# Kernel tuning notes

Hardware: AMD Instinct MI355X
Metric: run time of the kernel (lower is better)

The kernel has to match this reference:

```python
import jax, jax.numpy as jnp
import numpy as np

N = 100000
E = 1600000
IN, HID, OUT = 128, 256, 47


def _glorot(key, shape):
    fan_in, fan_out = shape
    lim = np.sqrt(6.0 / (fan_in + fan_out))
    return jax.random.uniform(key, shape, jnp.float32, -lim, lim)


def setup_inputs() -> dict:
    key = jax.random.key(0)
    ks = jax.random.split(key, 12)
    x = jax.random.normal(ks[0], (N, IN), jnp.float32)
    src = jax.random.randint(ks[1], (E,), 0, N, jnp.int32)
    dst = jax.random.randint(ks[2], (E,), 0, N, jnp.int32)
    dims = [(IN, HID), (HID, HID), (HID, OUT)]
    inp = {"x": x, "src": src, "dst": dst}
    for i, (di, do) in enumerate(dims, 1):
        inp[f"w_self{i}"] = _glorot(ks[2 + 3 * i - 2], (di, do))
        inp[f"w_neigh{i}"] = _glorot(ks[2 + 3 * i - 1], (di, do))
        inp[f"b{i}"] = jnp.zeros((do,), jnp.float32)
    return inp


def sage_conv(x, src, dst, w_self, w_neigh, b):
    n = x.shape[0]
    msg = x[src]                                              # [E, d] gather
    summed = jax.ops.segment_sum(msg, dst, num_segments=n)    # [N, d]
    deg = jax.ops.segment_sum(jnp.ones((src.shape[0],), x.dtype), dst, num_segments=n)
    h_neigh = summed / jnp.maximum(deg, 1.0)[:, None]         # mean aggregate
    return x @ w_self + h_neigh @ w_neigh + b


def reference(x, src, dst, w_self1, w_neigh1, b1, w_self2, w_neigh2, b2, w_self3, w_neigh3, b3):
    h = sage_conv(x, src, dst, w_self1, w_neigh1, b1)
    h = jax.nn.relu(h)  # dropout = identity in eval mode
    h = sage_conv(h, src, dst, w_self2, w_neigh2, b2)
    h = jax.nn.relu(h)
    h = sage_conv(h, src, dst, w_self3, w_neigh3, b3)
    return h
```

## Files before the change

kernel.cpp:

```cpp
#include <hip/hip_runtime.h>

#define N_NODES 100000
#define N_EDGES 1600000

typedef __attribute__((ext_vector_type(8))) _Float16 half8;
typedef __attribute__((ext_vector_type(4))) _Float16 half4v;
typedef __attribute__((ext_vector_type(4))) float floatx4;


__global__ void deg_rank(const int* __restrict__ dst, int* __restrict__ deg,
                         int* __restrict__ rank, int e) {
    int i = blockIdx.x * blockDim.x + threadIdx.x;
    if (i < e) rank[i] = atomicAdd(&deg[dst[i]], 1);
}


__global__ __launch_bounds__(256) void scan_partial(const int* __restrict__ deg,
                                                    int* __restrict__ bsum, int n) {
    __shared__ int wsum[4];
    int t = threadIdx.x;
    int base = blockIdx.x * 2048 + t * 8;
    int tsum = 0;
    #pragma unroll
    for (int k = 0; k < 8; ++k) {
        int idx = base + k;
        tsum += (idx < n) ? deg[idx] : 0;
    }
    #pragma unroll
    for (int d = 1; d < 64; d <<= 1) tsum += __shfl_xor(tsum, d, 64);
    if ((t & 63) == 0) wsum[t >> 6] = tsum;
    __syncthreads();
    if (t == 0) bsum[blockIdx.x] = wsum[0] + wsum[1] + wsum[2] + wsum[3];
}

__global__ void scan_blocksums(const int* __restrict__ bsum, int* __restrict__ bbase, int nb) {
    int t = threadIdx.x;
    int v = (t < nb) ? bsum[t] : 0;
    int s = v;
    #pragma unroll
    for (int d = 1; d < 64; d <<= 1) {
        int u = __shfl_up(s, d, 64);
        if (t >= d) s += u;
    }
    if (t < nb) bbase[t] = s - v;
    if (t == 63) bbase[nb] = s;
}

__global__ __launch_bounds__(256) void scan_write(const int* __restrict__ deg,
                                                  const int* __restrict__ bbase,
                                                  int* __restrict__ offs, int n, int nb) {
    __shared__ int wsum[4];
    int t = threadIdx.x;
    int lane = t & 63, w = t >> 6;
    int base = blockIdx.x * 2048 + t * 8;
    int v[8];
    #pragma unroll
    for (int k = 0; k < 8; ++k) {
        int idx = base + k;
        v[k] = (idx < n) ? deg[idx] : 0;
    }
    int tsum = 0;
    #pragma unroll
    for (int k = 0; k < 8; ++k) { int x = v[k]; v[k] = tsum; tsum += x; }
    int s = tsum;
    #pragma unroll
    for (int d = 1; d < 64; d <<= 1) {
        int u = __shfl_up(s, d, 64);
        if (lane >= d) s += u;
    }
    if (lane == 63) wsum[w] = s;
    __syncthreads();
    int wb = 0;
    for (int j = 0; j < w; ++j) wb += wsum[j];
    int texcl = bbase[blockIdx.x] + wb + (s - tsum);
    #pragma unroll
    for (int k = 0; k < 8; ++k) {
        int idx = base + k;
        if (idx < n) offs[idx] = texcl + v[k];
    }
    if (blockIdx.x == 0 && t == 0) offs[n] = bbase[nb];
}

__global__ void fill_csr2(const int* __restrict__ src, const int* __restrict__ dst,
                          const int* __restrict__ offs, const int* __restrict__ rank,
                          int* __restrict__ csr, int e) {
    int i = blockIdx.x * blockDim.x + threadIdx.x;
    if (i < e) csr[offs[dst[i]] + rank[i]] = src[i];
}


__global__ void cvt_f16(const float4* __restrict__ in, half4v* __restrict__ oh, int n4) {
    int i = blockIdx.x * blockDim.x + threadIdx.x;
    if (i >= n4) return;
    float4 v = in[i];
    half4v h;
    h[0] = (_Float16)v.x; h[1] = (_Float16)v.y;
    h[2] = (_Float16)v.z; h[3] = (_Float16)v.w;
    oh[i] = h;
}


__global__ void prep_all(const float* __restrict__ ws1, const float* __restrict__ wn1,
                         const float* __restrict__ ws2, const float* __restrict__ wn2,
                         const float* __restrict__ ws3, const float* __restrict__ wn3,
                         _Float16* __restrict__ o1s, _Float16* __restrict__ o1n,
                         _Float16* __restrict__ o2s, _Float16* __restrict__ o2n,
                         _Float16* __restrict__ o3c) {
    int i = blockIdx.x * blockDim.x + threadIdx.x;
    if (i < 65536) {
        const float* W = (i < 32768) ? ws1 : wn1;
        _Float16* O = (i < 32768) ? o1s : o1n;
        int j = i & 32767;
        int nn = j >> 7, k = j & 127;
        O[j] = (_Float16)W[k * 256 + nn];
    } else if (i < 196608) {
        int j = i - 65536;
        const float* W = (j < 65536) ? ws2 : wn2;
        _Float16* O = (j < 65536) ? o2s : o2n;
        j &= 65535;
        int nn = j >> 8, k = j & 255;
        O[j] = (_Float16)W[k * 256 + nn];
    } else if (i < 221184) {
        int j = i - 196608;
        const float* W = (j < 12288) ? ws3 : wn3;
        _Float16* O = o3c + ((j < 12288) ? 0 : 12288);
        j = (j < 12288) ? j : j - 12288;
        int nn = j >> 8, k = j & 255;
        O[j] = (nn < 47) ? (_Float16)W[k * 47 + nn] : (_Float16)0.f;
    }
}


__global__ __launch_bounds__(256) void aggP(const _Float16* __restrict__ Xp,
                                            const int* __restrict__ csr,
                                            const int* __restrict__ offs,
                                            _Float16* __restrict__ Pp, int n) {
    int node = blockIdx.x * 4 + (threadIdx.x >> 6);
    int lane = threadIdx.x & 63;
    int qtr = lane >> 4;
    int sl = lane & 15;
    if (node >= n) return;
    int e0 = offs[node], e1 = offs[node + 1];
    float a[8] = {0.f, 0.f, 0.f, 0.f, 0.f, 0.f, 0.f, 0.f};
    int e = e0;
    for (; e + 16 <= e1; e += 16) {
        int s0 = csr[e + qtr];
        int s1 = csr[e + 4 + qtr];
        int s2 = csr[e + 8 + qtr];
        int s3 = csr[e + 12 + qtr];
        half8 u0 = ((const half8*)(Xp + (size_t)s0 * 128))[sl];
        half8 u1 = ((const half8*)(Xp + (size_t)s1 * 128))[sl];
        half8 u2 = ((const half8*)(Xp + (size_t)s2 * 128))[sl];
        half8 u3 = ((const half8*)(Xp + (size_t)s3 * 128))[sl];
        #pragma unroll
        for (int j = 0; j < 8; ++j) a[j] += (float)u0[j];
        #pragma unroll
        for (int j = 0; j < 8; ++j) a[j] += (float)u1[j];
        #pragma unroll
        for (int j = 0; j < 8; ++j) a[j] += (float)u2[j];
        #pragma unroll
        for (int j = 0; j < 8; ++j) a[j] += (float)u3[j];
    }
    for (; e + 8 <= e1; e += 8) {
        int s0 = csr[e + qtr];
        int s1 = csr[e + 4 + qtr];
        half8 u0 = ((const half8*)(Xp + (size_t)s0 * 128))[sl];
        half8 u1 = ((const half8*)(Xp + (size_t)s1 * 128))[sl];
        #pragma unroll
        for (int j = 0; j < 8; ++j) a[j] += (float)u0[j];
        #pragma unroll
        for (int j = 0; j < 8; ++j) a[j] += (float)u1[j];
    }
    for (; e + 4 <= e1; e += 4) {
        int s = csr[e + qtr];
        half8 u = ((const half8*)(Xp + (size_t)s * 128))[sl];
        #pragma unroll
        for (int j = 0; j < 8; ++j) a[j] += (float)u[j];
    }
    int rem = e1 - e;
    if (qtr < rem) {
        int s = csr[e + qtr];
        half8 u = ((const half8*)(Xp + (size_t)s * 128))[sl];
        #pragma unroll
        for (int j = 0; j < 8; ++j) a[j] += (float)u[j];
    }
    #pragma unroll
    for (int j = 0; j < 8; ++j) {
        a[j] += __shfl_xor(a[j], 16);
        a[j] += __shfl_xor(a[j], 32);
    }
    if (lane < 16) {
        float inv = 1.0f / fmaxf((float)(e1 - e0), 1.0f);
        half8 rh;
        #pragma unroll
        for (int j = 0; j < 8; ++j) rh[j] = (_Float16)(a[j] * inv);
        ((half8*)(Pp + (size_t)node * 128))[sl] = rh;
    }
}

__global__ __launch_bounds__(256) void agg_l3(const _Float16* __restrict__ Y,
                                              const float* __restrict__ S,
                                              const int* __restrict__ csr,
                                              const int* __restrict__ offs,
                                              float* __restrict__ out, int n) {
    int node = blockIdx.x * 4 + (threadIdx.x >> 6);
    int lane = threadIdx.x & 63;
    int qtr = lane >> 4;
    int sl = lane & 15;
    int c = sl < 12 ? sl : 11;
    if (node >= n) return;
    int e0 = offs[node], e1 = offs[node + 1];
    float a0 = 0.f, a1 = 0.f, a2 = 0.f, a3 = 0.f;
    int e = e0;
    for (; e + 8 <= e1; e += 8) {
        int s0 = csr[e + qtr];
        int s1 = csr[e + 4 + qtr];
        half4v f0 = ((const half4v*)(Y + (size_t)s0 * 48))[c];
        half4v f1 = ((const half4v*)(Y + (size_t)s1 * 48))[c];
        a0 += (float)f0[0] + (float)f1[0];
        a1 += (float)f0[1] + (float)f1[1];
        a2 += (float)f0[2] + (float)f1[2];
        a3 += (float)f0[3] + (float)f1[3];
    }
    for (; e + 4 <= e1; e += 4) {
        int s = csr[e + qtr];
        half4v f = ((const half4v*)(Y + (size_t)s * 48))[c];
        a0 += (float)f[0]; a1 += (float)f[1]; a2 += (float)f[2]; a3 += (float)f[3];
    }
    int rem = e1 - e;
    if (qtr < rem) {
        int s = csr[e + qtr];
        half4v f = ((const half4v*)(Y + (size_t)s * 48))[c];
        a0 += (float)f[0]; a1 += (float)f[1]; a2 += (float)f[2]; a3 += (float)f[3];
    }
    a0 += __shfl_xor(a0, 16); a0 += __shfl_xor(a0, 32);
    a1 += __shfl_xor(a1, 16); a1 += __shfl_xor(a1, 32);
    a2 += __shfl_xor(a2, 16); a2 += __shfl_xor(a2, 32);
    a3 += __shfl_xor(a3, 16); a3 += __shfl_xor(a3, 32);
    if (lane < 12) {
        float inv = 1.0f / fmaxf((float)(e1 - e0), 1.0f);
        float4 sv = ((const float4*)(S + (size_t)node * 48))[c];
        float r[4] = {sv.x + a0 * inv, sv.y + a1 * inv, sv.z + a2 * inv, sv.w + a3 * inv};
        #pragma unroll
        for (int k = 0; k < 4; ++k) {
            int col = c * 4 + k;
            if (col < 47) out[(size_t)node * 47 + col] = r[k];
        }
    }
}


template <int NTILES, int OUTFMT>
__global__ __launch_bounds__(256, 2) void gemm_mfma(
    const _Float16* __restrict__ A1h, const _Float16* __restrict__ A2h,
    const _Float16* __restrict__ W1, const _Float16* __restrict__ W2,
    const float* __restrict__ bias, float* __restrict__ outS, _Float16* __restrict__ outY,
    _Float16* __restrict__ outh, int n, int K, int dout, int relu, int phases) {
    constexpr int NPAD = NTILES * 16;
    constexpr int LDT = 36;
    __shared__ _Float16 Bs[2][NPAD * LDT];

    const int t = threadIdx.x;
    const int bm = blockIdx.x * 128;
    const int lane = t & 63;
    const int w = t >> 6;
    const int quad = lane >> 4;
    const int tl = lane & 15;
    const int r0 = bm + w * 32 + tl;
    const int r1 = r0 + 16;
    const size_t PS = (size_t)n * 128;

    floatx4 acc[2][NTILES];
    #pragma unroll
    for (int i = 0; i < 2; ++i)
        #pragma unroll
        for (int j = 0; j < NTILES; ++j) acc[i][j] = (floatx4){0.f, 0.f, 0.f, 0.f};

    const int spp = K >> 5;
    const int nsteps = phases * spp;

    half8 pb0, pb1, pb2, pb3;
    half8 a0A = {0}, a1A = {0}, a0B = {0}, a1B = {0};

    auto wload = [&](int s2) {
        int ph2 = (s2 >= spp) ? 1 : 0;
        int k02 = (ph2 ? s2 - spp : s2) << 5;
        const _Float16* W = ph2 ? W2 : W1;
        const half8* p = (const half8*)(W + (size_t)t * K + k02);
        pb0 = p[0]; pb1 = p[1]; pb2 = p[2]; pb3 = p[3];
    };
    auto aload = [&](int s2, half8& d0, half8& d1) {
        int ph2 = (s2 >= spp) ? 1 : 0;
        int k02 = (ph2 ? s2 - spp : s2) << 5;
        const _Float16* Ah = ph2 ? A2h : A1h;
        int kq = k02 + quad * 8;
        const _Float16* Ab = Ah + ((kq >> 7) ? PS : (size_t)0) + (kq & 127);
        d0 = (half8){0}; d1 = (half8){0};
        if (r0 < n) d0 = *(const half8*)(Ab + (size_t)r0 * 128);
        if (r1 < n) d1 = *(const half8*)(Ab + (size_t)r1 * 128);
    };

    if (t < NPAD) {
        wload(0);
        *(half8*)&Bs[0][t * LDT + 0]  = pb0;
        *(half8*)&Bs[0][t * LDT + 8]  = pb1;
        *(half8*)&Bs[0][t * LDT + 16] = pb2;
        *(half8*)&Bs[0][t * LDT + 24] = pb3;
        wload(1);
    }
    aload(0, a0A, a1A);
    aload(1, a0B, a1B);
    __syncthreads();

    for (int s = 0; s < nsteps; s += 2) {
        {
            if (s + 1 < nsteps && t < NPAD) {
                *(half8*)&Bs[1][t * LDT + 0]  = pb0;
                *(half8*)&Bs[1][t * LDT + 8]  = pb1;
                *(half8*)&Bs[1][t * LDT + 16] = pb2;
                *(half8*)&Bs[1][t * LDT + 24] = pb3;
                if (s + 2 < nsteps) wload(s + 2);
            }
            half8 ca0 = a0A, ca1 = a1A;
            if (s + 2 < nsteps) aload(s + 2, a0A, a1A);
            #pragma unroll
            for (int nt = 0; nt < NTILES; ++nt) {
                half8 bh = *(const half8*)&Bs[0][(nt * 16 + tl) * LDT + quad * 8];
                acc[0][nt] = __builtin_amdgcn_mfma_f32_16x16x32_f16(ca0, bh, acc[0][nt], 0, 0, 0);
                acc[1][nt] = __builtin_amdgcn_mfma_f32_16x16x32_f16(ca1, bh, acc[1][nt], 0, 0, 0);
            }
            asm volatile("s_waitcnt lgkmcnt(0)" ::: "memory");
            __builtin_amdgcn_sched_barrier(0);
            __builtin_amdgcn_s_barrier();
        }
        {
            int s1 = s + 1;
            if (s1 + 1 < nsteps && t < NPAD) {
                *(half8*)&Bs[0][t * LDT + 0]  = pb0;
                *(half8*)&Bs[0][t * LDT + 8]  = pb1;
                *(half8*)&Bs[0][t * LDT + 16] = pb2;
                *(half8*)&Bs[0][t * LDT + 24] = pb3;
                if (s1 + 2 < nsteps) wload(s1 + 2);
            }
            half8 ca0 = a0B, ca1 = a1B;
            if (s1 + 2 < nsteps) aload(s1 + 2, a0B, a1B);
            #pragma unroll
            for (int nt = 0; nt < NTILES; ++nt) {
                half8 bh = *(const half8*)&Bs[1][(nt * 16 + tl) * LDT + quad * 8];
                acc[0][nt] = __builtin_amdgcn_mfma_f32_16x16x32_f16(ca0, bh, acc[0][nt], 0, 0, 0);
                acc[1][nt] = __builtin_amdgcn_mfma_f32_16x16x32_f16(ca1, bh, acc[1][nt], 0, 0, 0);
            }
            asm volatile("s_waitcnt lgkmcnt(0)" ::: "memory");
            __builtin_amdgcn_sched_barrier(0);
            __builtin_amdgcn_s_barrier();
        }
    }

    #pragma unroll
    for (int mt = 0; mt < 2; ++mt) {
        #pragma unroll
        for (int nt = 0; nt < NTILES; ++nt) {
            int gc = nt * 16 + tl;
            if (OUTFMT == 1 && gc >= dout) continue;
            #pragma unroll
            for (int r = 0; r < 4; ++r) {
                int gr = bm + w * 32 + mt * 16 + quad * 4 + r;
                if (gr >= n) continue;
                float v = acc[mt][nt][r];
                if (OUTFMT == 1) {
                    v += bias[gc];
                    if (relu) v = fmaxf(v, 0.f);
                    outh[(size_t)(gc >> 7) * PS + (size_t)gr * 128 + (gc & 127)] = (_Float16)v;
                } else {
                    if (gc < 48) {
                        v += (gc < 47) ? bias[gc] : 0.f;
                        outS[(size_t)gr * 48 + gc] = v;
                    } else {
                        outY[(size_t)gr * 48 + (gc - 48)] = (_Float16)v;
                    }
                }
            }
        }
    }
}

extern "C" void kernel_launch(void* const* d_in, const int* in_sizes, int n_in,
                              void* d_out, int out_size, void* d_ws, size_t ws_size,
                              hipStream_t stream) {
    (void)in_sizes; (void)n_in; (void)out_size; (void)ws_size;
    const int N = N_NODES, E = N_EDGES;
    const float* x = (const float*)d_in[0];
    const int* src = (const int*)d_in[1];
    const int* dst = (const int*)d_in[2];
    const float* w_self1 = (const float*)d_in[3];
    const float* w_neigh1 = (const float*)d_in[4];
    const float* b1 = (const float*)d_in[5];
    const float* w_self2 = (const float*)d_in[6];
    const float* w_neigh2 = (const float*)d_in[7];
    const float* b2 = (const float*)d_in[8];
    const float* w_self3 = (const float*)d_in[9];
    const float* w_neigh3 = (const float*)d_in[10];
    const float* b3 = (const float*)d_in[11];
    float* out = (float*)d_out;

    _Float16* Ph = (_Float16*)d_ws;
    _Float16* Hh = Ph + (size_t)N * 256;
    int* deg = (int*)(Hh + (size_t)N * 256);
    int* offs = deg + N;
    int* csr = offs + N + 4;
    _Float16* wbuf = (_Float16*)(csr + E);
    _Float16* w1s = wbuf;
    _Float16* w1n = w1s + 32768;
    _Float16* w2s = w1n + 32768;
    _Float16* w2n = w2s + 65536;
    _Float16* w3c = w2n + 65536;
    int* bsum = (int*)(w3c + 24576);
    int* bbase = bsum + 64;
    int* rank = (int*)Ph;
    _Float16* xh = Ph + (size_t)N * 128;
    float* S = (float*)Ph;
    _Float16* Y = (_Float16*)(S + (size_t)N * 48);

    const int NB = (N + 2047) / 2048;

    hipMemsetAsync(deg, 0, N * sizeof(int), stream);
    deg_rank<<<(E + 255) / 256, 256, 0, stream>>>(dst, deg, rank, E);
    scan_partial<<<NB, 256, 0, stream>>>(deg, bsum, N);
    scan_blocksums<<<1, 64, 0, stream>>>(bsum, bbase, NB);
    scan_write<<<NB, 256, 0, stream>>>(deg, bbase, offs, N, NB);
    fill_csr2<<<(E + 255) / 256, 256, 0, stream>>>(src, dst, offs, rank, csr, E);

    cvt_f16<<<(N * 128 / 4 + 255) / 256, 256, 0, stream>>>((const float4*)x, (half4v*)xh,
                                                           N * 128 / 4);
    prep_all<<<(221184 + 255) / 256, 256, 0, stream>>>(w_self1, w_neigh1, w_self2, w_neigh2,
                                                       w_self3, w_neigh3, w1s, w1n, w2s, w2n,
                                                       w3c);

    int gemmGrid = (N + 127) / 128;
    int aggGrid = (N + 3) / 4;

    aggP<<<aggGrid, 256, 0, stream>>>(xh, csr, offs, Ph, N);
    gemm_mfma<16, 1><<<gemmGrid, 256, 0, stream>>>(xh, Ph, w1s, w1n, b1, nullptr, nullptr,
                                                   Hh, N, 128, 256, 1, 2);
    aggP<<<aggGrid, 256, 0, stream>>>(Hh, csr, offs, Ph, N);
    aggP<<<aggGrid, 256, 0, stream>>>(Hh + (size_t)N * 128, csr, offs, Ph + (size_t)N * 128, N);
    gemm_mfma<16, 1><<<gemmGrid, 256, 0, stream>>>(Hh, Ph, w2s, w2n, b2, nullptr, nullptr,
                                                   Hh, N, 256, 256, 1, 2);
    gemm_mfma<6, 2><<<gemmGrid, 256, 0, stream>>>(Hh, nullptr, w3c, nullptr, b3, S, Y,
                                                  nullptr, N, 256, 96, 0, 1);
    agg_l3<<<aggGrid, 256, 0, stream>>>(Y, S, csr, offs, out, N);
}
```

Measured before the change: 643.7 us.

## Add 64-row GEMM kernel with column-split grid and separate layer-2 output buffer

Adds a new MFMA GEMM kernel that tiles 64 rows per block and splits the output columns across a second grid dimension, so there are more, smaller blocks and a higher occupancy target. Layers 1 and 3 use it. For layer 2 it writes to a separate H2 buffer when the workspace is large enough, because column-split blocks cannot safely overwrite their own input in place. Otherwise it falls back to the old in-place kernel. The trade-off is that A tiles are re-read once per column split and fewer MFMAs are issued per A load.

New measurement: 601.0 us. 1.07x faster.

```diff
diff --git a/kernel.cpp b/kernel.cpp
--- a/kernel.cpp
+++ b/kernel.cpp
@@ -13,7 +13,6 @@
     int i = blockIdx.x * blockDim.x + threadIdx.x;
     if (i < e) rank[i] = atomicAdd(&deg[dst[i]], 1);
 }
-
 
 __global__ __launch_bounds__(256) void scan_partial(const int* __restrict__ deg,
                                                     int* __restrict__ bsum, int n) {
@@ -251,6 +250,130 @@
 
 
 template <int NTILES, int OUTFMT>
+__global__ __launch_bounds__(256, 3) void gemm64(
+    const _Float16* __restrict__ A1h, const _Float16* __restrict__ A2h,
+    const _Float16* __restrict__ W1, const _Float16* __restrict__ W2,
+    const float* __restrict__ bias, float* __restrict__ outS, _Float16* __restrict__ outY,
+    _Float16* __restrict__ outh, int n, int K, int relu, int phases) {
+    constexpr int NPAD = NTILES * 16;
+    constexpr int LDT = 36;
+    __shared__ _Float16 Bs[2][NPAD * LDT];
+
+    const int t = threadIdx.x;
+    const int bm = blockIdx.x * 64;
+    const int colbase = blockIdx.y * NPAD;
+    const int lane = t & 63;
+    const int w = t >> 6;
+    const int quad = lane >> 4;
+    const int tl = lane & 15;
+    const int r0 = bm + w * 16 + tl;
+    const size_t PS = (size_t)n * 128;
+
+    floatx4 acc[NTILES];
+    #pragma unroll
+    for (int j = 0; j < NTILES; ++j) acc[j] = (floatx4){0.f, 0.f, 0.f, 0.f};
+
+    const int spp = K >> 5;
+    const int nsteps = phases * spp;
+
+    const int tr = t >> 1;
+    const int koff = (t & 1) * 16;
+    const bool stager = (t < 2 * NPAD);
+
+    half8 pb0, pb1;
+    half8 aA = {0}, aB = {0};
+
+    auto wload = [&](int s2) {
+        int ph2 = (s2 >= spp) ? 1 : 0;
+        int k02 = (ph2 ? s2 - spp : s2) << 5;
+        const _Float16* W = ph2 ? W2 : W1;
+        const half8* p = (const half8*)(W + (size_t)(colbase + tr) * K + k02 + koff);
+        pb0 = p[0]; pb1 = p[1];
+    };
+    auto aload = [&](int s2, half8& d) {
+        int ph2 = (s2 >= spp) ? 1 : 0;
+        int k02 = (ph2 ? s2 - spp : s2) << 5;
+        const _Float16* Ah = ph2 ? A2h : A1h;
+        int kq = k02 + quad * 8;
+        const _Float16* Ab = Ah + ((kq >> 7) ? PS : (size_t)0) + (kq & 127);
+        d = (half8){0};
+        if (r0 < n) d = *(const half8*)(Ab + (size_t)r0 * 128);
+    };
+
+    if (stager) {
+        wload(0);
+        *(half8*)&Bs[0][tr * LDT + koff]     = pb0;
+        *(half8*)&Bs[0][tr * LDT + koff + 8] = pb1;
+        wload(1);
+    }
+    aload(0, aA);
+    aload(1, aB);
+    __syncthreads();
+
+    for (int s = 0; s < nsteps; s += 2) {
+        {
+            if (s + 1 < nsteps && stager) {
+                *(half8*)&Bs[1][tr * LDT + koff]     = pb0;
+                *(half8*)&Bs[1][tr * LDT + koff + 8] = pb1;
+                if (s + 2 < nsteps) wload(s + 2);
+            }
+            half8 ca = aA;
+            if (s + 2 < nsteps) aload(s + 2, aA);
+            #pragma unroll
+            for (int nt = 0; nt < NTILES; ++nt) {
+                half8 bh = *(const half8*)&Bs[0][(nt * 16 + tl) * LDT + quad * 8];
+                acc[nt] = __builtin_amdgcn_mfma_f32_16x16x32_f16(ca, bh, acc[nt], 0, 0, 0);
+            }
+            asm volatile("s_waitcnt lgkmcnt(0)" ::: "memory");
+            __builtin_amdgcn_sched_barrier(0);
+            __builtin_amdgcn_s_barrier();
+        }
+        {
+            int s1 = s + 1;
+            if (s1 + 1 < nsteps && stager) {
+                *(half8*)&Bs[0][tr * LDT + koff]     = pb0;
+                *(half8*)&Bs[0][tr * LDT + koff + 8] = pb1;
+                if (s1 + 2 < nsteps) wload(s1 + 2);
+            }
+            half8 ca = aB;
+            if (s1 + 2 < nsteps) aload(s1 + 2, aB);
+            #pragma unroll
+            for (int nt = 0; nt < NTILES; ++nt) {
+                half8 bh = *(const half8*)&Bs[1][(nt * 16 + tl) * LDT + quad * 8];
+                acc[nt] = __builtin_amdgcn_mfma_f32_16x16x32_f16(ca, bh, acc[nt], 0, 0, 0);
+            }
+            asm volatile("s_waitcnt lgkmcnt(0)" ::: "memory");
+            __builtin_amdgcn_sched_barrier(0);
+            __builtin_amdgcn_s_barrier();
+        }
+    }
+
+    #pragma unroll
+    for (int nt = 0; nt < NTILES; ++nt) {
+        int gc = colbase + nt * 16 + tl;
+        #pragma unroll
+        for (int r = 0; r < 4; ++r) {
+            int gr = bm + w * 16 + quad * 4 + r;
+            if (gr >= n) continue;
+            float v = acc[nt][r];
+            if (OUTFMT == 1) {
+                v += bias[gc];
+                if (relu) v = fmaxf(v, 0.f);
+                outh[(size_t)(gc >> 7) * PS + (size_t)gr * 128 + (gc & 127)] = (_Float16)v;
+            } else {
+                if (gc < 48) {
+                    v += (gc < 47) ? bias[gc] : 0.f;
+                    outS[(size_t)gr * 48 + gc] = v;
+                } else {
+                    outY[(size_t)gr * 48 + (gc - 48)] = (_Float16)v;
+                }
+            }
+        }
+    }
+}
+
+
+template <int NTILES, int OUTFMT>
 __global__ __launch_bounds__(256, 2) void gemm_mfma(
     const _Float16* __restrict__ A1h, const _Float16* __restrict__ A2h,
     const _Float16* __restrict__ W1, const _Float16* __restrict__ W2,
@@ -387,7 +510,7 @@
 extern "C" void kernel_launch(void* const* d_in, const int* in_sizes, int n_in,
                               void* d_out, int out_size, void* d_ws, size_t ws_size,
                               hipStream_t stream) {
-    (void)in_sizes; (void)n_in; (void)out_size; (void)ws_size;
+    (void)in_sizes; (void)n_in; (void)out_size;
     const int N = N_NODES, E = N_EDGES;
     const float* x = (const float*)d_in[0];
     const int* src = (const int*)d_in[1];
@@ -420,6 +543,10 @@
     _Float16* xh = Ph + (size_t)N * 128;
     float* S = (float*)Ph;
     _Float16* Y = (_Float16*)(S + (size_t)N * 48);
+    size_t used = (size_t)((char*)(bbase + 64) - (char*)d_ws);
+    used = (used + 255) & ~(size_t)255;
+    _Float16* H2 = (_Float16*)((char*)d_ws + used);
+    const bool dbuf = (used + (size_t)N * 256 * sizeof(_Float16)) <= ws_size;
 
     const int NB = (N + 2047) / 2048;
 
@@ -436,17 +563,25 @@
                                                        w_self3, w_neigh3, w1s, w1n, w2s, w2n,
                                                        w3c);
 
-    int gemmGrid = (N + 127) / 128;
+    const int g64 = (N + 63) / 64;
     int aggGrid = (N + 3) / 4;
 
     aggP<<<aggGrid, 256, 0, stream>>>(xh, csr, offs, Ph, N);
-    gemm_mfma<16, 1><<<gemmGrid, 256, 0, stream>>>(xh, Ph, w1s, w1n, b1, nullptr, nullptr,
-                                                   Hh, N, 128, 256, 1, 2);
+    gemm64<8, 1><<<dim3(g64, 2), 256, 0, stream>>>(xh, Ph, w1s, w1n, b1, nullptr, nullptr,
+                                                   Hh, N, 128, 1, 2);
     aggP<<<aggGrid, 256, 0, stream>>>(Hh, csr, offs, Ph, N);
     aggP<<<aggGrid, 256, 0, stream>>>(Hh + (size_t)N * 128, csr, offs, Ph + (size_t)N * 128, N);
-    gemm_mfma<16, 1><<<gemmGrid, 256, 0, stream>>>(Hh, Ph, w2s, w2n, b2, nullptr, nullptr,
-                                                   Hh, N, 256, 256, 1, 2);
-    gemm_mfma<6, 2><<<gemmGrid, 256, 0, stream>>>(Hh, nullptr, w3c, nullptr, b3, S, Y,
-                                                  nullptr, N, 256, 96, 0, 1);
+    const _Float16* Hcur;
+    if (dbuf) {
+        gemm64<8, 1><<<dim3(g64, 2), 256, 0, stream>>>(Hh, Ph, w2s, w2n, b2, nullptr, nullptr,
+                                                       H2, N, 256, 1, 2);
+        Hcur = H2;
+    } else {
+        gemm_mfma<16, 1><<<(N + 127) / 128, 256, 0, stream>>>(Hh, Ph, w2s, w2n, b2, nullptr,
+                                                              nullptr, Hh, N, 256, 256, 1, 2);
+        Hcur = Hh;
+    }
+    gemm64<6, 2><<<dim3(g64, 1), 256, 0, stream>>>(Hcur, nullptr, w3c, nullptr, b3, S, Y,
+                                                   nullptr, N, 256, 0, 1);
     agg_l3<<<aggGrid, 256, 0, stream>>>(Y, S, csr, offs, out, N);
 }
```
